# Performance work log

Measured on AMD Instinct MI355X. Metric: run time of the kernel, lower is better.

## Reference

```python
import jax, jax.numpy as jnp
import numpy as np

E = 1024      # embed_dim
QH = 16       # query heads
KVH = 4       # kv heads
HD = E // QH  # head_dim = 64
KVE = HD * KVH  # 256
EPS = 1e-5
ROPE_BASE = 10000.0


def rope(x, d):
    # Faithful to the source RoPE: d == number of heads (x.shape[-2]),
    # and the 'sequence' axis of the cache is x.shape[0] (the batch dim).
    # rope(x) = x*cos + (x*sin) * neg_half(x)  (note: nonlinear in x).
    b = x.shape[0]
    theta = 1.0 / (ROPE_BASE ** (jnp.arange(0, d, 2, dtype=jnp.float32) / d))  # (d//2,)
    seq_idx = jnp.arange(b, dtype=jnp.float32)                                 # (b,)
    idx_theta = seq_idx[:, None] * theta[None, :]                              # (b, d//2)
    idx2 = jnp.concatenate([idx_theta, idx_theta], axis=-1)                    # (b, d)
    # cached shape (b,1,1,d); source permutes (0,1,3,2) -> (b,1,d,1)
    cos = jnp.cos(idx2)[:, None, :, None]  # (b,1,d,1)
    sin = jnp.sin(idx2)[:, None, :, None]
    d2 = d // 2
    # split of the LAST dim (head_dim) at d//2 == num_heads//2, as in source
    neg = jnp.concatenate([-x[..., d2:], x[..., :d2]], axis=-1)
    return x * cos + (x * sin) * neg


def setup_inputs() -> dict:
    key = jax.random.key(0)
    ks = jax.random.split(key, 12)
    b, n = 1, 2048

    def xavier(k, shape):
        fan_out, fan_in = shape
        std = (2.0 / (fan_in + fan_out)) ** 0.5
        return jax.random.normal(k, shape, dtype=jnp.float32) * std

    return {
        "query": jax.random.normal(ks[0], (b, n, E), dtype=jnp.float32),
        "key": jax.random.normal(ks[1], (b, n, E), dtype=jnp.float32),
        "value": jax.random.normal(ks[2], (b, n, E), dtype=jnp.float32),
        "Wq": xavier(ks[3], (E, E)),
        "bq": jnp.zeros((E,), jnp.float32),
        "Wk": xavier(ks[4], (KVE, E)),
        "bk": jnp.zeros((KVE,), jnp.float32),
        "Wv": xavier(ks[5], (KVE, E)),
        "bv": jnp.zeros((KVE,), jnp.float32),
        "gamma": jnp.ones((E,), jnp.float32),
        "beta": jnp.zeros((E,), jnp.float32),
    }


def reference(query, key, value, Wq, bq, Wk, bk, Wv, bv, gamma, beta):
    b, n, _ = query.shape
    q = query @ Wq.T + bq            # (b,n,E)
    k = key @ Wk.T + bk              # (b,n,KVE)
    v = value @ Wv.T + bv            # (b,n,KVE)

    q = q.reshape(b, n, QH, HD)      # b n h d
    k = k.reshape(b, n, KVH, HD)
    v = v.reshape(b, n, KVH, HD)

    q = rope(q, QH)
    k = rope(k, KVH)

    # b n h d -> b h n d
    q = jnp.transpose(q, (0, 2, 1, 3))
    k = jnp.transpose(k, (0, 2, 1, 3))
    v = jnp.transpose(v, (0, 2, 1, 3))

    scale = float(HD) ** 0.5
    q = q / scale

    g = QH // KVH
    # 'b (h g) n d -> b g h n d' : h outer, g inner
    q = q.reshape(b, KVH, g, n, HD)              # (b, h, g, n, d)
    q = jnp.transpose(q, (0, 2, 1, 3, 4))        # (b, g, h, n, d)

    sim = jnp.einsum('bghnd,bhsd->bghns', q, k)  # (b,g,h,n,s)
    attn = jax.nn.softmax(sim, axis=-1)
    out = jnp.einsum('bghns,bhsd->bghnd', attn, v)

    # 'b g h n d -> b n (h g) d'
    out = jnp.transpose(out, (0, 3, 2, 1, 4))    # (b, n, h, g, d)
    x = out.reshape(b, n, QH * HD)               # (b, n, E)

    # LayerNorm (biased variance, as in torch)
    mu = jnp.mean(x, axis=-1, keepdims=True)
    var = jnp.mean((x - mu) ** 2, axis=-1, keepdims=True)
    x = (x - mu) * jax.lax.rsqrt(var + EPS) * gamma + beta

    # NOTE: source computes out_proj(x) but returns x, so out_proj is dead code.
    return x
```

## Files before the change

### kernel.cpp

```cpp
#include <hip/hip_runtime.h>
#include <math.h>

#define EDIM   1024
#define KVEDIM 256
#define HDIM   64
#define QHEADS 16
#define NSEG   2

typedef __attribute__((ext_vector_type(8))) short short8;
typedef __attribute__((ext_vector_type(4))) float f32x4;

__device__ __forceinline__ unsigned pack2(float a, float b) {
    unsigned ua = __builtin_bit_cast(unsigned, a);
    unsigned ub = __builtin_bit_cast(unsigned, b);
    ua += 0x7fffu + ((ua >> 16) & 1u);
    ub += 0x7fffu + ((ub >> 16) & 1u);
    return (ua >> 16) | (ub & 0xffff0000u);
}
__device__ __forceinline__ short f2b(float a) {
    unsigned ua = __builtin_bit_cast(unsigned, a);
    ua += 0x7fffu + ((ua >> 16) & 1u);
    return (short)(ua >> 16);
}

#if __has_builtin(__builtin_amdgcn_exp2f)
__device__ __forceinline__ float fexp2(float x) { return __builtin_amdgcn_exp2f(x); }
#else
__device__ __forceinline__ float fexp2(float x) { return exp2f(x); }
#endif

__global__ __launch_bounds__(256)
void proj_gemm(const float* __restrict__ Aq, const float* __restrict__ Ak,
               const float* __restrict__ Av,
               const float* __restrict__ Wq, const float* __restrict__ Wk,
               const float* __restrict__ Wv,
               const float* __restrict__ bq, const float* __restrict__ bk,
               const float* __restrict__ bv,
               short* __restrict__ Cq, short* __restrict__ Ck,
               short* __restrict__ Cv, float qscale)
{
    const int bid = blockIdx.x;
    const float* A; const float* W; const float* bias; short* C;
    int N, bm, bn; float scale;
    if (bid < 512) {
        A = Aq; W = Wq; bias = bq; C = Cq; N = EDIM; scale = qscale;
        bm = (bid >> 4) * 64; bn = (bid & 15) * 64;
    } else if (bid < 640) {
        int i = bid - 512;
        A = Ak; W = Wk; bias = bk; C = Ck; N = KVEDIM; scale = 1.0f;
        bm = (i >> 2) * 64; bn = (i & 3) * 64;
    } else {
        int i = bid - 640;
        A = Av; W = Wv; bias = bv; C = Cv; N = KVEDIM; scale = 1.0f;
        bm = (i >> 2) * 64; bn = (i & 3) * 64;
    }
    const int K = EDIM;

    __shared__ short As[64 * 136];
    __shared__ short Ws[64 * 136];

    const int t = threadIdx.x, lane = t & 63, wv = t >> 6;
    const int lm = lane & 15, quad = lane >> 4;
    const int q8 = quad * 8, q4 = quad * 4;
    const int wm = (wv & 1) * 32, wn = (wv >> 1) * 32;
    const int srow = t >> 5;
    const int scol = (t & 31) * 4;

    f32x4 zero = {0.f, 0.f, 0.f, 0.f};
    f32x4 acc[2][2];
    #pragma unroll
    for (int i = 0; i < 2; ++i)
        #pragma unroll
        for (int j = 0; j < 2; ++j) acc[i][j] = zero;

    for (int k0 = 0; k0 < K; k0 += 128) {
        __syncthreads();
        #pragma unroll
        for (int i = 0; i < 8; ++i) {
            int r = i * 8 + srow;
            float4 a = *(const float4*)&A[(size_t)(bm + r) * K + k0 + scol];
            uint2 pa; pa.x = pack2(a.x, a.y); pa.y = pack2(a.z, a.w);
            *(uint2*)&As[r * 136 + scol] = pa;
            float4 w = *(const float4*)&W[(size_t)(bn + r) * K + k0 + scol];
            uint2 pw; pw.x = pack2(w.x, w.y); pw.y = pack2(w.z, w.w);
            *(uint2*)&Ws[r * 136 + scol] = pw;
        }
        __syncthreads();
        #pragma unroll
        for (int ks = 0; ks < 4; ++ks) {
            short8 af[2], wf[2];
            #pragma unroll
            for (int i = 0; i < 2; ++i)
                af[i] = *(const short8*)&As[(wm + i * 16 + lm) * 136 + ks * 32 + q8];
            #pragma unroll
            for (int j = 0; j < 2; ++j)
                wf[j] = *(const short8*)&Ws[(wn + j * 16 + lm) * 136 + ks * 32 + q8];
            #pragma unroll
            for (int i = 0; i < 2; ++i)
                #pragma unroll
                for (int j = 0; j < 2; ++j)
                    acc[i][j] = __builtin_amdgcn_mfma_f32_16x16x32_bf16(
                        af[i], wf[j], acc[i][j], 0, 0, 0);
        }
    }

    #pragma unroll
    for (int j = 0; j < 2; ++j) {
        float bj = bias[bn + wn + j * 16 + lm];
        #pragma unroll
        for (int i = 0; i < 2; ++i)
            #pragma unroll
            for (int r = 0; r < 4; ++r)
                C[(size_t)(bm + wm + i * 16 + q4 + r) * N + bn + wn + j * 16 + lm] =
                    f2b((acc[i][j][r] + bj) * scale);
    }
}

__global__ __launch_bounds__(256)
void attn_mfma(const short* __restrict__ q, const short* __restrict__ k,
               const short* __restrict__ v, float* __restrict__ Opart,
               float* __restrict__ Lpart, int n)
{
    __shared__ short Ks[64 * 72];
    __shared__ short Vt[64 * 72];
    __shared__ short Ps[64 * 72];
    __shared__ float Lred[4][64];

    const int qh = blockIdx.y, kvh = qh >> 2;
    const int r0 = blockIdx.x * 64;
    const int seg = blockIdx.z;
    const int segkeys = n / NSEG;
    const int sbeg = seg * segkeys;
    const int t = threadIdx.x;
    const int lane = t & 63, wv = t >> 6;
    const int lm = lane & 15, quad = lane >> 4;
    const int q8 = quad * 8, q4 = quad * 4;

    short8 qf[4][2];
    #pragma unroll
    for (int qt = 0; qt < 4; ++qt) {
        const short* qrow = &q[(size_t)(r0 + qt * 16 + lm) * EDIM + qh * HDIM];
        qf[qt][0] = *(const short8*)&qrow[q8];
        qf[qt][1] = *(const short8*)&qrow[32 + q8];
    }

    const int rt0 = (wv & 1) * 2;
    const int dt0 = (wv >> 1) * 2;

    f32x4 zero = {0.f, 0.f, 0.f, 0.f};
    f32x4 oacc[2][2];
    #pragma unroll
    for (int i = 0; i < 2; ++i)
        #pragma unroll
        for (int j = 0; j < 2; ++j) oacc[i][j] = zero;
    float lp[4] = {0.f, 0.f, 0.f, 0.f};

    const int krow = t >> 2, kc = (t & 3) * 8;
    const int vs4 = (t & 15) * 4, vd0 = (t >> 4) * 4;

    for (int c = 0; c < segkeys; c += 64) {
        const int s0 = sbeg + c;
        __syncthreads();
        {
            const uint4* ksrc = (const uint4*)&k[(size_t)(s0 + krow) * KVEDIM + kvh * HDIM];
            uint4 ka = ksrc[t & 3];
            uint4 kb = ksrc[(t & 3) + 4];
            *(uint4*)&Ks[krow * 72 + kc] = ka;
            *(uint4*)&Ks[krow * 72 + kc + 32] = kb;
        }
        {
            unsigned vr[4][2];
            #pragma unroll
            for (int i = 0; i < 4; ++i) {
                uint2 vv = *(const uint2*)&v[(size_t)(s0 + vs4 + i) * KVEDIM + kvh * HDIM + vd0];
                vr[i][0] = vv.x; vr[i][1] = vv.y;
            }
            #pragma unroll
            for (int j = 0; j < 4; ++j) {
                int w = j >> 1, hi = (j & 1) * 16;
                unsigned e0 = (vr[0][w] >> hi) & 0xffffu;
                unsigned e1 = (vr[1][w] >> hi) & 0xffffu;
                unsigned e2 = (vr[2][w] >> hi) & 0xffffu;
                unsigned e3 = (vr[3][w] >> hi) & 0xffffu;
                uint2 o; o.x = e0 | (e1 << 16); o.y = e2 | (e3 << 16);
                *(uint2*)&Vt[(vd0 + j) * 72 + vs4] = o;
            }
        }
        __syncthreads();

        short8 kf0 = *(const short8*)&Ks[(wv * 16 + lm) * 72 + q8];
        short8 kf1 = *(const short8*)&Ks[(wv * 16 + lm) * 72 + 32 + q8];
        #pragma unroll
        for (int qt = 0; qt < 4; ++qt) {
            f32x4 s = zero;
            s = __builtin_amdgcn_mfma_f32_16x16x32_bf16(kf0, qf[qt][0], s, 0, 0, 0);
            s = __builtin_amdgcn_mfma_f32_16x16x32_bf16(kf1, qf[qt][1], s, 0, 0, 0);
            float p0 = fexp2(s[0]);
            float p1 = fexp2(s[1]);
            float p2 = fexp2(s[2]);
            float p3 = fexp2(s[3]);
            lp[qt] += (p0 + p1) + (p2 + p3);
            uint2 pw; pw.x = pack2(p0, p1); pw.y = pack2(p2, p3);
            *(uint2*)&Ps[(qt * 16 + lm) * 72 + wv * 16 + q4] = pw;
        }
        __syncthreads();

        short8 vf[2][2];
        #pragma unroll
        for (int j = 0; j < 2; ++j) {
            vf[j][0] = *(const short8*)&Vt[((dt0 + j) * 16 + lm) * 72 + q8];
            vf[j][1] = *(const short8*)&Vt[((dt0 + j) * 16 + lm) * 72 + 32 + q8];
        }
        #pragma unroll
        for (int i = 0; i < 2; ++i) {
            short8 pf0 = *(const short8*)&Ps[((rt0 + i) * 16 + lm) * 72 + q8];
            short8 pf1 = *(const short8*)&Ps[((rt0 + i) * 16 + lm) * 72 + 32 + q8];
            #pragma unroll
            for (int j = 0; j < 2; ++j) {
                oacc[i][j] = __builtin_amdgcn_mfma_f32_16x16x32_bf16(pf0, vf[j][0], oacc[i][j], 0, 0, 0);
                oacc[i][j] = __builtin_amdgcn_mfma_f32_16x16x32_bf16(pf1, vf[j][1], oacc[i][j], 0, 0, 0);
            }
        }
    }

    #pragma unroll
    for (int qt = 0; qt < 4; ++qt) {
        float l = lp[qt];
        l += __shfl_xor(l, 16);
        l += __shfl_xor(l, 32);
        if (lane < 16) Lred[wv][qt * 16 + lm] = l;
    }
    __syncthreads();

    #pragma unroll
    for (int i = 0; i < 2; ++i) {
        #pragma unroll
        for (int r = 0; r < 4; ++r) {
            int row = (rt0 + i) * 16 + q4 + r;
            float lsum = (Lred[0][row] + Lred[1][row]) + (Lred[2][row] + Lred[3][row]);
            if (dt0 == 0 && lm == 0)
                Lpart[((size_t)seg * n + r0 + row) * QHEADS + qh] = lsum;
            #pragma unroll
            for (int j = 0; j < 2; ++j)
                Opart[((size_t)seg * n + r0 + row) * EDIM + qh * HDIM + (dt0 + j) * 16 + lm] =
                    oacc[i][j][r];
        }
    }
}

__global__ __launch_bounds__(256)
void combine_ln(const float* __restrict__ Opart, const float* __restrict__ Lpart,
                const float* __restrict__ gamma, const float* __restrict__ beta,
                float* __restrict__ out, int n)
{
    const int r = blockIdx.x;
    const int t = threadIdx.x;

    __shared__ float linv[QHEADS];
    if (t < QHEADS) {
        float l = 0.f;
        #pragma unroll
        for (int s = 0; s < NSEG; ++s)
            l += Lpart[((size_t)s * n + r) * QHEADS + t];
        linv[t] = 1.0f / l;
    }
    __syncthreads();

    const int c = t * 4;
    float4 o = {0.f, 0.f, 0.f, 0.f};
    #pragma unroll
    for (int s = 0; s < NSEG; ++s) {
        float4 p = *(const float4*)&Opart[((size_t)s * n + r) * EDIM + c];
        o.x += p.x; o.y += p.y; o.z += p.z; o.w += p.w;
    }
    const float inv = linv[c >> 6];
    o.x *= inv; o.y *= inv; o.z *= inv; o.w *= inv;

    float s  = o.x + o.y + o.z + o.w;
    float sq = o.x * o.x + o.y * o.y + o.z * o.z + o.w * o.w;
    #pragma unroll
    for (int m = 1; m < 64; m <<= 1) {
        s  += __shfl_xor(s,  m);
        sq += __shfl_xor(sq, m);
    }
    __shared__ float ws_[4], wq_[4];
    const int wave = t >> 6;
    if ((t & 63) == 0) { ws_[wave] = s; wq_[wave] = sq; }
    __syncthreads();
    s  = ws_[0] + ws_[1] + ws_[2] + ws_[3];
    sq = wq_[0] + wq_[1] + wq_[2] + wq_[3];

    const float mu   = s * (1.f / EDIM);
    const float var  = sq * (1.f / EDIM) - mu * mu;
    const float rstd = rsqrtf(var + 1e-5f);

    float4 g = *(const float4*)&gamma[c];
    float4 b = *(const float4*)&beta[c];
    float4 y;
    y.x = (o.x - mu) * rstd * g.x + b.x;
    y.y = (o.y - mu) * rstd * g.y + b.y;
    y.z = (o.z - mu) * rstd * g.z + b.z;
    y.w = (o.w - mu) * rstd * g.w + b.w;
    *(float4*)&out[(size_t)r * EDIM + c] = y;
}

extern "C" void kernel_launch(void* const* d_in, const int* in_sizes, int n_in,
                              void* d_out, int out_size, void* d_ws, size_t ws_size,
                              hipStream_t stream)
{
    const float* query = (const float*)d_in[0];
    const float* key   = (const float*)d_in[1];
    const float* value = (const float*)d_in[2];
    const float* Wq    = (const float*)d_in[3];
    const float* bq    = (const float*)d_in[4];
    const float* Wk    = (const float*)d_in[5];
    const float* bk    = (const float*)d_in[6];
    const float* Wv    = (const float*)d_in[7];
    const float* bv    = (const float*)d_in[8];
    const float* gamma = (const float*)d_in[9];
    const float* beta  = (const float*)d_in[10];
    float* out = (float*)d_out;

    const int n = in_sizes[0] / EDIM;

    short* qb = (short*)d_ws;
    short* kb = qb + (size_t)n * EDIM;
    short* vb = kb + (size_t)n * KVEDIM;
    float* Opart = (float*)(vb + (size_t)n * KVEDIM);
    float* Lpart = Opart + (size_t)NSEG * n * EDIM;

    const float qscale = 0.125f * 1.44269504088896f;

    proj_gemm<<<dim3(768), 256, 0, stream>>>(
        query, key, value, Wq, Wk, Wv, bq, bk, bv, qb, kb, vb, qscale);

    attn_mfma<<<dim3(n / 64, QHEADS, NSEG), 256, 0, stream>>>(
        qb, kb, vb, Opart, Lpart, n);

    combine_ln<<<dim3(n), 256, 0, stream>>>(Opart, Lpart, gamma, beta, out, n);
}
```

Measured before the change: 188.1 us.

## Pre-convert inputs to bf16, enlarge GEMM tiles, pre-transpose V, per-wave attention

Adds a separate pass that converts the inputs and weights to bf16 up front. The projection GEMM now works on 64x128 tiles with a 64-wide K step and register prefetch of the next slice. A new kernel writes a transposed copy of V to global memory. The attention kernel is rewritten so each wave owns 16 query rows and loads K and V fragments straight from global memory, dropping the shared K/V staging and the block-wide barriers. This costs two extra launches plus extra global traffic for the bf16 copies and the transposed V, in exchange for less in-kernel conversion work and less synchronisation.

```diff
diff --git a/kernel.cpp b/kernel.cpp
--- a/kernel.cpp
+++ b/kernel.cpp
@@ -30,82 +30,125 @@
 #endif
 
 __global__ __launch_bounds__(256)
-void proj_gemm(const float* __restrict__ Aq, const float* __restrict__ Ak,
-               const float* __restrict__ Av,
-               const float* __restrict__ Wq, const float* __restrict__ Wk,
-               const float* __restrict__ Wv,
+void cvt_bf16(const float* __restrict__ query, const float* __restrict__ key,
+              const float* __restrict__ value,
+              const float* __restrict__ Wq, const float* __restrict__ Wk,
+              const float* __restrict__ Wv,
+              short* __restrict__ qa, short* __restrict__ ka, short* __restrict__ va,
+              short* __restrict__ wqb, short* __restrict__ wkb, short* __restrict__ wvb,
+              int n)
+{
+    const int base = ((int)blockIdx.x * 256 + (int)threadIdx.x) * 8;
+    const int stride = (int)gridDim.x * 256 * 8;
+    auto cvt_one = [&](const float* __restrict__ s, short* __restrict__ d, int nn) {
+        for (int i = base; i < nn; i += stride) {
+            float4 x = *(const float4*)&s[i];
+            float4 y = *(const float4*)&s[i + 4];
+            uint4 o;
+            o.x = pack2(x.x, x.y); o.y = pack2(x.z, x.w);
+            o.z = pack2(y.x, y.y); o.w = pack2(y.z, y.w);
+            *(uint4*)&d[i] = o;
+        }
+    };
+    cvt_one(query, qa, n * EDIM);
+    cvt_one(key,   ka, n * EDIM);
+    cvt_one(value, va, n * EDIM);
+    cvt_one(Wq, wqb, EDIM * EDIM);
+    cvt_one(Wk, wkb, KVEDIM * EDIM);
+    cvt_one(Wv, wvb, KVEDIM * EDIM);
+}
+
+__global__ __launch_bounds__(256)
+void proj_gemm(const short* __restrict__ qa, const short* __restrict__ ka,
+               const short* __restrict__ va,
+               const short* __restrict__ wqb, const short* __restrict__ wkb,
+               const short* __restrict__ wvb,
                const float* __restrict__ bq, const float* __restrict__ bk,
                const float* __restrict__ bv,
-               short* __restrict__ Cq, short* __restrict__ Ck,
-               short* __restrict__ Cv, float qscale)
-{
-    const int bid = blockIdx.x;
-    const float* A; const float* W; const float* bias; short* C;
-    int N, bm, bn; float scale;
-    if (bid < 512) {
-        A = Aq; W = Wq; bias = bq; C = Cq; N = EDIM; scale = qscale;
-        bm = (bid >> 4) * 64; bn = (bid & 15) * 64;
-    } else if (bid < 640) {
-        int i = bid - 512;
-        A = Ak; W = Wk; bias = bk; C = Ck; N = KVEDIM; scale = 1.0f;
-        bm = (i >> 2) * 64; bn = (i & 3) * 64;
-    } else {
-        int i = bid - 640;
-        A = Av; W = Wv; bias = bv; C = Cv; N = KVEDIM; scale = 1.0f;
-        bm = (i >> 2) * 64; bn = (i & 3) * 64;
-    }
-    const int K = EDIM;
-
-    __shared__ short As[64 * 136];
-    __shared__ short Ws[64 * 136];
-
-    const int t = threadIdx.x, lane = t & 63, wv = t >> 6;
+               short* __restrict__ qb, short* __restrict__ kb,
+               short* __restrict__ vb, float qscale)
+{
+    __shared__ __align__(16) short sm[13824];
+    const int t = threadIdx.x, lane = t & 63, wvv = t >> 6;
     const int lm = lane & 15, quad = lane >> 4;
     const int q8 = quad * 8, q4 = quad * 4;
-    const int wm = (wv & 1) * 32, wn = (wv >> 1) * 32;
-    const int srow = t >> 5;
-    const int scol = (t & 31) * 4;
-
-    f32x4 zero = {0.f, 0.f, 0.f, 0.f};
-    f32x4 acc[2][2];
+    const int wm = (wvv & 1) * 32, wn = (wvv >> 1) * 64;
+
+    short* As = sm;
+    short* Ws = sm + 4608;
+
+    const int ar = t >> 2, acol = (t & 3) * 16;
+    const int wr = t >> 1, wcol = (t & 1) * 32;
+
+    const int tile = blockIdx.x;
+    const short* A; const short* W; const float* bias; short* C;
+    int N, bm, bn; float scale;
+    if (tile < 256) {
+        A = qa; W = wqb; bias = bq; C = qb; N = EDIM; scale = qscale;
+        bm = (tile >> 3) * 64; bn = (tile & 7) * 128;
+    } else if (tile < 320) {
+        int i = tile - 256;
+        A = ka; W = wkb; bias = bk; C = kb; N = KVEDIM; scale = 1.0f;
+        bm = (i >> 1) * 64; bn = (i & 1) * 128;
+    } else {
+        int i = tile - 320;
+        A = va; W = wvb; bias = bv; C = vb; N = KVEDIM; scale = 1.0f;
+        bm = (i >> 1) * 64; bn = (i & 1) * 128;
+    }
+
+    const short* Ab = A + (size_t)(bm + ar) * EDIM + acol;
+    const short* Wb = W + (size_t)(bn + wr) * EDIM + wcol;
+
+    f32x4 acc[2][4];
     #pragma unroll
     for (int i = 0; i < 2; ++i)
         #pragma unroll
-        for (int j = 0; j < 2; ++j) acc[i][j] = zero;
-
-    for (int k0 = 0; k0 < K; k0 += 128) {
+        for (int j = 0; j < 4; ++j) acc[i][j] = {0.f, 0.f, 0.f, 0.f};
+
+    uint4 pa0 = *(const uint4*)(Ab);
+    uint4 pa1 = *(const uint4*)(Ab + 8);
+    uint4 pw0 = *(const uint4*)(Wb);
+    uint4 pw1 = *(const uint4*)(Wb + 8);
+    uint4 pw2 = *(const uint4*)(Wb + 16);
+    uint4 pw3 = *(const uint4*)(Wb + 24);
+
+    for (int k0 = 0; k0 < EDIM; k0 += 64) {
         __syncthreads();
-        #pragma unroll
-        for (int i = 0; i < 8; ++i) {
-            int r = i * 8 + srow;
-            float4 a = *(const float4*)&A[(size_t)(bm + r) * K + k0 + scol];
-            uint2 pa; pa.x = pack2(a.x, a.y); pa.y = pack2(a.z, a.w);
-            *(uint2*)&As[r * 136 + scol] = pa;
-            float4 w = *(const float4*)&W[(size_t)(bn + r) * K + k0 + scol];
-            uint2 pw; pw.x = pack2(w.x, w.y); pw.y = pack2(w.z, w.w);
-            *(uint2*)&Ws[r * 136 + scol] = pw;
-        }
+        *(uint4*)&As[ar * 72 + acol]      = pa0;
+        *(uint4*)&As[ar * 72 + acol + 8]  = pa1;
+        *(uint4*)&Ws[wr * 72 + wcol]      = pw0;
+        *(uint4*)&Ws[wr * 72 + wcol + 8]  = pw1;
+        *(uint4*)&Ws[wr * 72 + wcol + 16] = pw2;
+        *(uint4*)&Ws[wr * 72 + wcol + 24] = pw3;
         __syncthreads();
-        #pragma unroll
-        for (int ks = 0; ks < 4; ++ks) {
-            short8 af[2], wf[2];
+        if (k0 + 64 < EDIM) {
+            pa0 = *(const uint4*)(Ab + k0 + 64);
+            pa1 = *(const uint4*)(Ab + k0 + 72);
+            pw0 = *(const uint4*)(Wb + k0 + 64);
+            pw1 = *(const uint4*)(Wb + k0 + 72);
+            pw2 = *(const uint4*)(Wb + k0 + 80);
+            pw3 = *(const uint4*)(Wb + k0 + 88);
+        }
+        #pragma unroll
+        for (int ks = 0; ks < 2; ++ks) {
+            short8 af[2], wf[4];
             #pragma unroll
             for (int i = 0; i < 2; ++i)
-                af[i] = *(const short8*)&As[(wm + i * 16 + lm) * 136 + ks * 32 + q8];
+                af[i] = *(const short8*)&As[(wm + i * 16 + lm) * 72 + ks * 32 + q8];
             #pragma unroll
-            for (int j = 0; j < 2; ++j)
-                wf[j] = *(const short8*)&Ws[(wn + j * 16 + lm) * 136 + ks * 32 + q8];
+            for (int j = 0; j < 4; ++j)
+                wf[j] = *(const short8*)&Ws[(wn + j * 16 + lm) * 72 + ks * 32 + q8];
             #pragma unroll
             for (int i = 0; i < 2; ++i)
                 #pragma unroll
-                for (int j = 0; j < 2; ++j)
+                for (int j = 0; j < 4; ++j)
                     acc[i][j] = __builtin_amdgcn_mfma_f32_16x16x32_bf16(
                         af[i], wf[j], acc[i][j], 0, 0, 0);
         }
     }
 
     #pragma unroll
-    for (int j = 0; j < 2; ++j) {
+    for (int j = 0; j < 4; ++j) {
         float bj = bias[bn + wn + j * 16 + lm];
         #pragma unroll
         for (int i = 0; i < 2; ++i)
@@ -117,135 +160,107 @@
 }
 
 __global__ __launch_bounds__(256)
-void attn_mfma(const short* __restrict__ q, const short* __restrict__ k,
-               const short* __restrict__ v, float* __restrict__ Opart,
+void vt_kernel(const short* __restrict__ vb, short* __restrict__ vt, int n)
+{
+    const int t = threadIdx.x;
+    const int s4 = ((int)blockIdx.x & 31) * 64 + (t & 15) * 4;
+    const int c4 = ((int)blockIdx.x >> 5) * 64 + (t >> 4) * 4;
+
+    uint2 vr[4];
+    #pragma unroll
+    for (int i = 0; i < 4; ++i)
+        vr[i] = *(const uint2*)&vb[(size_t)(s4 + i) * KVEDIM + c4];
+    #pragma unroll
+    for (int j = 0; j < 4; ++j) {
+        int w = j >> 1, hi = (j & 1) * 16;
+        unsigned e0 = (vr[0].x * (w == 0) + vr[0].y * (w == 1)) ;
+        unsigned a0 = w ? vr[0].y : vr[0].x;
+        unsigned a1 = w ? vr[1].y : vr[1].x;
+        unsigned a2 = w ? vr[2].y : vr[2].x;
+        unsigned a3 = w ? vr[3].y : vr[3].x;
+        unsigned f0 = (a0 >> hi) & 0xffffu;
+        unsigned f1 = (a1 >> hi) & 0xffffu;
+        unsigned f2 = (a2 >> hi) & 0xffffu;
+        unsigned f3 = (a3 >> hi) & 0xffffu;
+        uint2 o; o.x = f0 | (f1 << 16); o.y = f2 | (f3 << 16);
+        *(uint2*)&vt[(size_t)(c4 + j) * n + s4] = o;
+        (void)e0;
+    }
+}
+
+__global__ __launch_bounds__(256, 4)
+void attn_wave(const short* __restrict__ qb, const short* __restrict__ kb,
+               const short* __restrict__ vt, float* __restrict__ Opart,
                float* __restrict__ Lpart, int n)
 {
-    __shared__ short Ks[64 * 72];
-    __shared__ short Vt[64 * 72];
-    __shared__ short Ps[64 * 72];
-    __shared__ float Lred[4][64];
-
+    __shared__ __align__(16) short Ps[4 * 16 * 72];
+
+    const int t = threadIdx.x, lane = t & 63, wv = t >> 6;
+    const int lm = lane & 15, quad = lane >> 4;
+    const int q8 = quad * 8, q4 = quad * 4;
     const int qh = blockIdx.y, kvh = qh >> 2;
-    const int r0 = blockIdx.x * 64;
     const int seg = blockIdx.z;
     const int segkeys = n / NSEG;
     const int sbeg = seg * segkeys;
-    const int t = threadIdx.x;
-    const int lane = t & 63, wv = t >> 6;
-    const int lm = lane & 15, quad = lane >> 4;
-    const int q8 = quad * 8, q4 = quad * 4;
-
-    short8 qf[4][2];
-    #pragma unroll
-    for (int qt = 0; qt < 4; ++qt) {
-        const short* qrow = &q[(size_t)(r0 + qt * 16 + lm) * EDIM + qh * HDIM];
-        qf[qt][0] = *(const short8*)&qrow[q8];
-        qf[qt][1] = *(const short8*)&qrow[32 + q8];
-    }
-
-    const int rt0 = (wv & 1) * 2;
-    const int dt0 = (wv >> 1) * 2;
+    const int row0 = (int)blockIdx.x * 64 + wv * 16;
+
+    short* Psw = Ps + wv * (16 * 72);
+
+    const short* qrowp = &qb[(size_t)(row0 + lm) * EDIM + qh * HDIM];
+    short8 qf0 = *(const short8*)&qrowp[q8];
+    short8 qf1 = *(const short8*)&qrowp[32 + q8];
 
     f32x4 zero = {0.f, 0.f, 0.f, 0.f};
-    f32x4 oacc[2][2];
-    #pragma unroll
-    for (int i = 0; i < 2; ++i)
-        #pragma unroll
-        for (int j = 0; j < 2; ++j) oacc[i][j] = zero;
-    float lp[4] = {0.f, 0.f, 0.f, 0.f};
-
-    const int krow = t >> 2, kc = (t & 3) * 8;
-    const int vs4 = (t & 15) * 4, vd0 = (t >> 4) * 4;
+    f32x4 oacc[4] = {zero, zero, zero, zero};
+    float lp = 0.f;
 
     for (int c = 0; c < segkeys; c += 64) {
         const int s0 = sbeg + c;
-        __syncthreads();
-        {
-            const uint4* ksrc = (const uint4*)&k[(size_t)(s0 + krow) * KVEDIM + kvh * HDIM];
-            uint4 ka = ksrc[t & 3];
-            uint4 kb = ksrc[(t & 3) + 4];
-            *(uint4*)&Ks[krow * 72 + kc] = ka;
-            *(uint4*)&Ks[krow * 72 + kc + 32] = kb;
-        }
-        {
-            unsigned vr[4][2];
-            #pragma unroll
-            for (int i = 0; i < 4; ++i) {
-                uint2 vv = *(const uint2*)&v[(size_t)(s0 + vs4 + i) * KVEDIM + kvh * HDIM + vd0];
-                vr[i][0] = vv.x; vr[i][1] = vv.y;
-            }
-            #pragma unroll
-            for (int j = 0; j < 4; ++j) {
-                int w = j >> 1, hi = (j & 1) * 16;
-                unsigned e0 = (vr[0][w] >> hi) & 0xffffu;
-                unsigned e1 = (vr[1][w] >> hi) & 0xffffu;
-                unsigned e2 = (vr[2][w] >> hi) & 0xffffu;
-                unsigned e3 = (vr[3][w] >> hi) & 0xffffu;
-                uint2 o; o.x = e0 | (e1 << 16); o.y = e2 | (e3 << 16);
-                *(uint2*)&Vt[(vd0 + j) * 72 + vs4] = o;
-            }
-        }
-        __syncthreads();
-
-        short8 kf0 = *(const short8*)&Ks[(wv * 16 + lm) * 72 + q8];
-        short8 kf1 = *(const short8*)&Ks[(wv * 16 + lm) * 72 + 32 + q8];
-        #pragma unroll
-        for (int qt = 0; qt < 4; ++qt) {
+
+        short8 kf[4][2];
+        #pragma unroll
+        for (int nt = 0; nt < 4; ++nt) {
+            const short* kr = &kb[(size_t)(s0 + nt * 16 + lm) * KVEDIM + kvh * HDIM];
+            kf[nt][0] = *(const short8*)&kr[q8];
+            kf[nt][1] = *(const short8*)&kr[32 + q8];
+        }
+        #pragma unroll
+        for (int nt = 0; nt < 4; ++nt) {
             f32x4 s = zero;
-            s = __builtin_amdgcn_mfma_f32_16x16x32_bf16(kf0, qf[qt][0], s, 0, 0, 0);
-            s = __builtin_amdgcn_mfma_f32_16x16x32_bf16(kf1, qf[qt][1], s, 0, 0, 0);
+            s = __builtin_amdgcn_mfma_f32_16x16x32_bf16(kf[nt][0], qf0, s, 0, 0, 0);
+            s = __builtin_amdgcn_mfma_f32_16x16x32_bf16(kf[nt][1], qf1, s, 0, 0, 0);
             float p0 = fexp2(s[0]);
             float p1 = fexp2(s[1]);
             float p2 = fexp2(s[2]);
             float p3 = fexp2(s[3]);
-            lp[qt] += (p0 + p1) + (p2 + p3);
+            lp += (p0 + p1) + (p2 + p3);
             uint2 pw; pw.x = pack2(p0, p1); pw.y = pack2(p2, p3);
-            *(uint2*)&Ps[(qt * 16 + lm) * 72 + wv * 16 + q4] = pw;
-        }
-        __syncthreads();
-
-        short8 vf[2][2];
-        #pragma unroll
-        for (int j = 0; j < 2; ++j) {
-            vf[j][0] = *(const short8*)&Vt[((dt0 + j) * 16 + lm) * 72 + q8];
-            vf[j][1] = *(const short8*)&Vt[((dt0 + j) * 16 + lm) * 72 + 32 + q8];
-        }
-        #pragma unroll
-        for (int i = 0; i < 2; ++i) {
-            short8 pf0 = *(const short8*)&Ps[((rt0 + i) * 16 + lm) * 72 + q8];
-            short8 pf1 = *(const short8*)&Ps[((rt0 + i) * 16 + lm) * 72 + 32 + q8];
-            #pragma unroll
-            for (int j = 0; j < 2; ++j) {
-                oacc[i][j] = __builtin_amdgcn_mfma_f32_16x16x32_bf16(pf0, vf[j][0], oacc[i][j], 0, 0, 0);
-                oacc[i][j] = __builtin_amdgcn_mfma_f32_16x16x32_bf16(pf1, vf[j][1], oacc[i][j], 0, 0, 0);
-            }
-        }
-    }
-
-    #pragma unroll
-    for (int qt = 0; qt < 4; ++qt) {
-        float l = lp[qt];
-        l += __shfl_xor(l, 16);
-        l += __shfl_xor(l, 32);
-        if (lane < 16) Lred[wv][qt * 16 + lm] = l;
-    }
-    __syncthreads();
-
-    #pragma unroll
-    for (int i = 0; i < 2; ++i) {
-        #pragma unroll
-        for (int r = 0; r < 4; ++r) {
-            int row = (rt0 + i) * 16 + q4 + r;
-            float lsum = (Lred[0][row] + Lred[1][row]) + (Lred[2][row] + Lred[3][row]);
-            if (dt0 == 0 && lm == 0)
-                Lpart[((size_t)seg * n + r0 + row) * QHEADS + qh] = lsum;
-            #pragma unroll
-            for (int j = 0; j < 2; ++j)
-                Opart[((size_t)seg * n + r0 + row) * EDIM + qh * HDIM + (dt0 + j) * 16 + lm] =
-                    oacc[i][j][r];
-        }
-    }
+            *(uint2*)&Psw[lm * 72 + nt * 16 + q4] = pw;
+        }
+
+        short8 pf0 = *(const short8*)&Psw[lm * 72 + q8];
+        short8 pf1 = *(const short8*)&Psw[lm * 72 + 32 + q8];
+        #pragma unroll
+        for (int dt = 0; dt < 4; ++dt) {
+            const short* vr = &vt[(size_t)(kvh * HDIM + dt * 16 + lm) * n + s0];
+            short8 vf0 = *(const short8*)&vr[q8];
+            short8 vf1 = *(const short8*)&vr[32 + q8];
+            oacc[dt] = __builtin_amdgcn_mfma_f32_16x16x32_bf16(pf0, vf0, oacc[dt], 0, 0, 0);
+            oacc[dt] = __builtin_amdgcn_mfma_f32_16x16x32_bf16(pf1, vf1, oacc[dt], 0, 0, 0);
+        }
+    }
+
+    lp += __shfl_xor(lp, 16);
+    lp += __shfl_xor(lp, 32);
+    if (quad == 0)
+        Lpart[((size_t)seg * n + row0 + lm) * QHEADS + qh] = lp;
+
+    #pragma unroll
+    for (int dt = 0; dt < 4; ++dt)
+        #pragma unroll
+        for (int r = 0; r < 4; ++r)
+            Opart[((size_t)seg * n + row0 + q4 + r) * EDIM + qh * HDIM + dt * 16 + lm] =
+                oacc[dt][r];
 }
 
 __global__ __launch_bounds__(256)
@@ -321,21 +336,33 @@
     const float* beta  = (const float*)d_in[10];
     float* out = (float*)d_out;
 
-    const int n = in_sizes[0] / EDIM;
-
-    short* qb = (short*)d_ws;
-    short* kb = qb + (size_t)n * EDIM;
-    short* vb = kb + (size_t)n * KVEDIM;
-    float* Opart = (float*)(vb + (size_t)n * KVEDIM);
+    int n = in_sizes[0] / EDIM;
+
+    short* qa  = (short*)d_ws;
+    short* ka  = qa  + (size_t)n * EDIM;
+    short* va  = ka  + (size_t)n * EDIM;
+    short* wqb = va  + (size_t)n * EDIM;
+    short* wkb = wqb + (size_t)EDIM * EDIM;
+    short* wvb = wkb + (size_t)KVEDIM * EDIM;
+    short* qb  = wvb + (size_t)KVEDIM * EDIM;
+    short* kb  = qb  + (size_t)n * EDIM;
+    short* vb  = kb  + (size_t)n * KVEDIM;
+    short* vtw = vb  + (size_t)n * KVEDIM;
+    float* Opart = (float*)(vtw + (size_t)KVEDIM * n);
     float* Lpart = Opart + (size_t)NSEG * n * EDIM;
 
-    const float qscale = 0.125f * 1.44269504088896f;
-
-    proj_gemm<<<dim3(768), 256, 0, stream>>>(
-        query, key, value, Wq, Wk, Wv, bq, bk, bv, qb, kb, vb, qscale);
-
-    attn_mfma<<<dim3(n / 64, QHEADS, NSEG), 256, 0, stream>>>(
-        qb, kb, vb, Opart, Lpart, n);
+    float qscale = 0.125f * 1.44269504088896f;
+
+    cvt_bf16<<<dim3(512), 256, 0, stream>>>(query, key, value, Wq, Wk, Wv,
+                                            qa, ka, va, wqb, wkb, wvb, n);
+
+    proj_gemm<<<dim3(384), 256, 0, stream>>>(qa, ka, va, wqb, wkb, wvb,
+                                             bq, bk, bv, qb, kb, vb, qscale);
+
+    vt_kernel<<<dim3((n / 64) * 4), 256, 0, stream>>>(vb, vtw, n);
+
+    attn_wave<<<dim3(n / 64, QHEADS, NSEG), 256, 0, stream>>>(
+        qb, kb, vtw, Opart, Lpart, n);
 
     combine_ln<<<dim3(n), 256, 0, stream>>>(Opart, Lpart, gamma, beta, out, n);
 }
```

Result: slower. 235.8 us (+25.3%).
